# Optimization experiments

Measured on AMD Instinct MI355X. Metric: run time of the kernel, lower is better.

The kernel has to match this reference:

```python
import jax, jax.numpy as jnp
import numpy as np

NUM_HEADS = 16
HEAD_DIM = 64
D_MODEL = 1024
OUTPUT_DIM = 1024


def setup_inputs() -> dict:
    key = jax.random.key(0)
    ks = jax.random.split(key, 11)
    B, S, H = 2, 2048, D_MODEL
    inner = NUM_HEADS * HEAD_DIM
    s = 0.02
    return {
        "query": jax.random.normal(ks[0], (B, S, H), jnp.float32),
        "key": jax.random.normal(ks[1], (B, S, H), jnp.float32),
        "value": jax.random.normal(ks[2], (B, S, H), jnp.float32),
        "Wq": jax.random.normal(ks[3], (H, inner), jnp.float32) * s,
        "bq": jnp.zeros((inner,), jnp.float32),
        "Wk": jax.random.normal(ks[4], (H, inner), jnp.float32) * s,
        "bk": jnp.zeros((inner,), jnp.float32),
        "Wv": jax.random.normal(ks[5], (H, inner), jnp.float32) * s,
        "bv": jnp.zeros((inner,), jnp.float32),
        "Wo": jax.random.normal(ks[6], (inner, OUTPUT_DIM), jnp.float32) * s,
        "bo": jnp.zeros((OUTPUT_DIM,), jnp.float32),
    }


def reference(query, key, value, Wq, bq, Wk, bk, Wv, bv, Wo, bo):
    B, Sq, _ = query.shape
    Sk = key.shape[1]
    nh, dh = NUM_HEADS, HEAD_DIM
    # projections -> [B, S, nh, dh]
    Q = (query @ Wq + bq).reshape(B, Sq, nh, dh)
    K = (key @ Wk + bk).reshape(B, Sk, nh, dh)
    V = (value @ Wv + bv).reshape(B, Sk, nh, dh)
    # scores [B, nh, Sq, Sk]
    scores = jnp.einsum("bqhd,bkhd->bhqk", Q, K) / jnp.sqrt(jnp.float32(dh))
    attn = jax.nn.softmax(scores, axis=-1)
    out = jnp.einsum("bhqk,bkhd->bqhd", attn, V).reshape(B, Sq, nh * dh)
    return out @ Wo + bo
```

## Files before the change

kernel.cpp:

```cpp
#include <hip/hip_runtime.h>
#include <math.h>

typedef __attribute__((ext_vector_type(8))) short short8;
typedef __attribute__((ext_vector_type(4))) short short4v;
typedef __attribute__((ext_vector_type(4))) float f32x4;
typedef __attribute__((ext_vector_type(2))) float f32x2;

#if __has_builtin(__builtin_amdgcn_mfma_f32_16x16x16bf16_1k)
#define HAVE_MFMA16 1
#else
#define HAVE_MFMA16 0
#endif

__device__ __forceinline__ short f2bf(float f) {
  union { float f; unsigned u; } x; x.f = f;
  unsigned r = x.u + 0x7fffu + ((x.u >> 16) & 1u);
  return (short)(r >> 16);
}
#if __has_builtin(__builtin_amdgcn_cvt_pk_bf16_f32)
typedef __attribute__((ext_vector_type(2))) __bf16 bf16x2;
__device__ __forceinline__ unsigned pack_bf(float a, float b) {
  union { bf16x2 v; unsigned u; } t;
  t.v = __builtin_amdgcn_cvt_pk_bf16_f32(a, b);
  return t.u;
}
#else
__device__ __forceinline__ unsigned pack_bf(float a, float b) {
  union { float f; unsigned u; } x, y; x.f = a; y.f = b;
  unsigned ra = x.u + 0x7fffu + ((x.u >> 16) & 1u);
  unsigned rb = y.u + 0x7fffu + ((y.u >> 16) & 1u);
  return (ra >> 16) | (rb & 0xffff0000u);
}
#endif
__device__ __forceinline__ float fast_exp2(float x) {
#if __has_builtin(__builtin_amdgcn_exp2f)
  return __builtin_amdgcn_exp2f(x);
#else
  return exp2f(x);
#endif
}
union U4S8 { unsigned u[4]; short8 s; };
union U2S4 { unsigned u[2]; short4v s; };

__device__ __forceinline__ void async16(const short* g, short* lds_uniform) {
  __builtin_amdgcn_global_load_lds(
      (const __attribute__((address_space(1))) void*)g,
      (__attribute__((address_space(3))) void*)lds_uniform, 16, 0, 0);
}

__global__ __launch_bounds__(256) void wconv(
    const float* __restrict__ W0, const float* __restrict__ W1,
    const float* __restrict__ W2, const float* __restrict__ W3,
    short* __restrict__ T0, short* __restrict__ T1,
    short* __restrict__ T2, short* __restrict__ T3) {
  const float* W; short* T;
  switch (blockIdx.z) {
    case 0: W = W0; T = T0; break;
    case 1: W = W1; T = T1; break;
    case 2: W = W2; T = T2; break;
    default: W = W3; T = T3; break;
  }
  __shared__ __align__(16) short t[64][72];
  const int tid = threadIdx.x;
  const int x0 = blockIdx.x * 64, y0 = blockIdx.y * 64;
  {
    int rr = tid >> 2, cc = (tid & 3) * 16;
    const float* p = W + (size_t)(x0 + rr) * 1024 + y0 + cc;
    f32x4 v[4];
    v[0] = *(const f32x4*)(p + 0);  v[1] = *(const f32x4*)(p + 4);
    v[2] = *(const f32x4*)(p + 8);  v[3] = *(const f32x4*)(p + 12);
#pragma unroll
    for (int i = 0; i < 4; ++i)
#pragma unroll
      for (int j = 0; j < 4; ++j)
        t[cc + 4 * i + j][rr] = f2bf(v[i][j]);
  }
  __syncthreads();
  {
    int nr = tid >> 2, kc = (tid & 3) * 16;
    short* q = T + (size_t)(y0 + nr) * 1024 + x0 + kc;
    *(short8*)q       = *(const short8*)&t[nr][kc];
    *(short8*)(q + 8) = *(const short8*)&t[nr][kc + 8];
  }
}

__global__ __launch_bounds__(256) void aconv(
    const float* __restrict__ X0, const float* __restrict__ X1, const float* __restrict__ X2,
    short* __restrict__ Y0, short* __restrict__ Y1, short* __restrict__ Y2) {
  const float* X; short* Y;
  switch (blockIdx.z) {
    case 0: X = X0; Y = Y0; break;
    case 1: X = X1; Y = Y1; break;
    default: X = X2; Y = Y2; break;
  }
  size_t idx = ((size_t)blockIdx.x * 256 + threadIdx.x) * 16;
  f32x4 v0 = *(const f32x4*)(X + idx + 0);
  f32x4 v1 = *(const f32x4*)(X + idx + 4);
  f32x4 v2 = *(const f32x4*)(X + idx + 8);
  f32x4 v3 = *(const f32x4*)(X + idx + 12);
  U4S8 a, b;
  a.u[0] = pack_bf(v0[0], v0[1]); a.u[1] = pack_bf(v0[2], v0[3]);
  a.u[2] = pack_bf(v1[0], v1[1]); a.u[3] = pack_bf(v1[2], v1[3]);
  b.u[0] = pack_bf(v2[0], v2[1]); b.u[1] = pack_bf(v2[2], v2[3]);
  b.u[2] = pack_bf(v3[0], v3[1]); b.u[3] = pack_bf(v3[2], v3[3]);
  *(short8*)(Y + idx) = a.s;
  *(short8*)(Y + idx + 8) = b.s;
}

template <bool OUT_F32, int BM>
__global__ __launch_bounds__(256) void gemm_async(
    const short* __restrict__ A0, const short* __restrict__ A1, const short* __restrict__ A2,
    const short* __restrict__ B0, const short* __restrict__ B1, const short* __restrict__ B2,
    const float* __restrict__ b0, const float* __restrict__ b1, const float* __restrict__ b2,
    void* __restrict__ C0, void* __restrict__ C1, void* __restrict__ C2,
    float s0, float s1, float s2, int M, int N, int K) {
  const int z = blockIdx.z;
  const short* A    = z == 0 ? A0 : (z == 1 ? A1 : A2);
  const short* B    = z == 0 ? B0 : (z == 1 ? B1 : B2);
  const float* bias = z == 0 ? b0 : (z == 1 ? b1 : b2);
  void*        Cv   = z == 0 ? C0 : (z == 1 ? C1 : C2);
  const float  cs   = z == 0 ? s0 : (z == 1 ? s1 : s2);

  constexpr int MF = BM / 32;
  constexpr int AJ = BM / 64;
  __shared__ __align__(16) short As[BM * 32];
  __shared__ __align__(16) short Bs[128 * 32];
  const int tid = threadIdx.x;
  const int l = tid & 63, w = tid >> 6;
  const int lr = l & 15, lq = l >> 4;
  const int lin = blockIdx.x + (int)gridDim.x * blockIdx.y;
  const int ny = (int)gridDim.y;
  const int yb = lin % ny, xb = lin / ny;
  const int m0 = yb * BM, n0 = xb * 128;
  const int wm = (w >> 1) * (BM / 2), wn = (w & 1) * 64;
  f32x4 acc[MF][4] = {};

  const int lrow = l >> 2, lcol = (l & 3) * 8;
  const short* aptr[AJ];
  short* alds[AJ];
#pragma unroll
  for (int j = 0; j < AJ; ++j) {
    int chunk = w * AJ + j;
    aptr[j] = A + (size_t)(m0 + chunk * 16 + lrow) * K + lcol;
    alds[j] = &As[chunk * 512];
  }
  const short* bptr[2];
  short* blds[2];
#pragma unroll
  for (int j = 0; j < 2; ++j) {
    int chunk = w * 2 + j;
    bptr[j] = B + (size_t)(n0 + chunk * 16 + lrow) * K + lcol;
    blds[j] = &Bs[chunk * 512];
  }

  const int KT = K >> 5;
  for (int kt = 0; kt < KT; ++kt) {
    const int k0 = kt * 32;
    __syncthreads();
#pragma unroll
    for (int j = 0; j < AJ; ++j) async16(aptr[j] + k0, alds[j]);
#pragma unroll
    for (int j = 0; j < 2; ++j) async16(bptr[j] + k0, blds[j]);
    __syncthreads();

    short8 af[MF], bfr[4];
#pragma unroll
    for (int i = 0; i < MF; ++i)
      af[i] = *(const short8*)&As[(wm + i * 16 + lr) * 32 + lq * 8];
#pragma unroll
    for (int i = 0; i < 4; ++i)
      bfr[i] = *(const short8*)&Bs[(wn + i * 16 + lr) * 32 + lq * 8];
#pragma unroll
    for (int mi = 0; mi < MF; ++mi)
#pragma unroll
      for (int ni = 0; ni < 4; ++ni)
        acc[mi][ni] = __builtin_amdgcn_mfma_f32_16x16x32_bf16(af[mi], bfr[ni], acc[mi][ni], 0, 0, 0);
  }

#pragma unroll
  for (int ni = 0; ni < 4; ++ni) {
    int gn = n0 + wn + ni * 16 + lr;
    float bv = bias[gn];
#pragma unroll
    for (int mi = 0; mi < MF; ++mi) {
      int gm = m0 + wm + mi * 16 + lq * 4;
#pragma unroll
      for (int r = 0; r < 4; ++r) {
        float val = (acc[mi][ni][r] + bv) * cs;
        if constexpr (OUT_F32)
          ((float*)Cv)[(size_t)(gm + r) * N + gn] = val;
        else
          ((short*)Cv)[(size_t)(gm + r) * N + gn] = f2bf(val);
      }
    }
  }
}

template <bool A_IS_F32, bool B_IS_BF16, bool OUT_F32, int BM>
__global__ __launch_bounds__(256) void gemm_bias(
    const void* __restrict__ A0, const void* __restrict__ A1, const void* __restrict__ A2,
    const void* __restrict__ B0, const void* __restrict__ B1, const void* __restrict__ B2,
    const float* __restrict__ b0, const float* __restrict__ b1, const float* __restrict__ b2,
    void* __restrict__ C0, void* __restrict__ C1, void* __restrict__ C2,
    float s0, float s1, float s2, int M, int N, int K) {
  const int z = blockIdx.z;
  const void*  Av   = z == 0 ? A0 : (z == 1 ? A1 : A2);
  const void*  Bv   = z == 0 ? B0 : (z == 1 ? B1 : B2);
  const float* bias = z == 0 ? b0 : (z == 1 ? b1 : b2);
  void*        Cv   = z == 0 ? C0 : (z == 1 ? C1 : C2);
  const float  cs   = z == 0 ? s0 : (z == 1 ? s1 : s2);

  constexpr int MF = BM / 32;
  __shared__ __align__(16) short As[BM * 40];
  __shared__ __align__(16) short Bs[128 * 40];
  const int tid = threadIdx.x;
  const int l = tid & 63, w = tid >> 6;
  const int lr = l & 15, lq = l >> 4;
  const int lin = blockIdx.x + (int)gridDim.x * blockIdx.y;
  const int ny = (int)gridDim.y;
  const int yb = lin % ny, xb = lin / ny;
  const int m0 = yb * BM, n0 = xb * 128;
  const int wm = (w >> 1) * (BM / 2), wn = (w & 1) * 64;
  f32x4 acc[MF][4] = {};

  constexpr int TPR = 256 / BM;
  const int ar = tid / TPR, ac = (tid % TPR) * (32 / TPR);
  const int br = tid >> 1, bcc = (tid & 1) * 16;
  const int dp = tid & 63, kb = tid >> 6;

  f32x4 avf[MF];
  short8 avb[BM / 64 > 0 ? BM / 64 : 1];
  short8 bvb[2];
  f32x2 bvf[8];

  auto load_regs = [&](int k0) {
    if constexpr (A_IS_F32) {
      const float* Ap = (const float*)Av + (size_t)(m0 + ar) * K + k0 + ac;
#pragma unroll
      for (int i = 0; i < MF; ++i) avf[i] = *(const f32x4*)(Ap + 4 * i);
    } else {
      const short* Ap = (const short*)Av + (size_t)(m0 + ar) * K + k0 + ac;
#pragma unroll
      for (int i = 0; i < BM / 64; ++i) avb[i] = *(const short8*)(Ap + 8 * i);
    }
    if constexpr (B_IS_BF16) {
      const short* Bp = (const short*)Bv + (size_t)(n0 + br) * K + k0 + bcc;
      bvb[0] = *(const short8*)(Bp + 0);
      bvb[1] = *(const short8*)(Bp + 8);
    } else {
      const float* Bp = (const float*)Bv + (size_t)(k0 + kb * 8) * N + n0 + 2 * dp;
#pragma unroll
      for (int i = 0; i < 4; ++i) {
        bvf[2 * i]     = *(const f32x2*)(Bp + (size_t)(2 * i) * N);
        bvf[2 * i + 1] = *(const f32x2*)(Bp + (size_t)(2 * i + 1) * N);
      }
    }
  };
  auto write_lds = [&]() {
    if constexpr (A_IS_F32) {
#pragma unroll
      for (int j = 0; j < MF / 2; ++j) {
        U4S8 p;
        p.u[0] = pack_bf(avf[2 * j][0], avf[2 * j][1]);
        p.u[1] = pack_bf(avf[2 * j][2], avf[2 * j][3]);
        p.u[2] = pack_bf(avf[2 * j + 1][0], avf[2 * j + 1][1]);
        p.u[3] = pack_bf(avf[2 * j + 1][2], avf[2 * j + 1][3]);
        *(short8*)&As[ar * 40 + ac + 8 * j] = p.s;
      }
    } else {
#pragma unroll
      for (int j = 0; j < BM / 64; ++j)
        *(short8*)&As[ar * 40 + ac + 8 * j] = avb[j];
    }
    if constexpr (B_IS_BF16) {
      *(short8*)&Bs[br * 40 + bcc] = bvb[0];
      *(short8*)&Bs[br * 40 + bcc + 8] = bvb[1];
    } else {
      U4S8 lo, hi;
#pragma unroll
      for (int i = 0; i < 4; ++i) {
        lo.u[i] = pack_bf(bvf[2 * i][0], bvf[2 * i + 1][0]);
        hi.u[i] = pack_bf(bvf[2 * i][1], bvf[2 * i + 1][1]);
      }
      *(short8*)&Bs[(2 * dp) * 40 + kb * 8] = lo.s;
      *(short8*)&Bs[(2 * dp + 1) * 40 + kb * 8] = hi.s;
    }
  };

  load_regs(0);
  const int KT = K >> 5;
  for (int kt = 0; kt < KT; ++kt) {
    write_lds();
    __syncthreads();
    if (kt + 1 < KT) load_regs((kt + 1) * 32);

    short8 af[MF], bfr[4];
#pragma unroll
    for (int i = 0; i < MF; ++i)
      af[i] = *(const short8*)&As[(wm + i * 16 + lr) * 40 + lq * 8];
#pragma unroll
    for (int i = 0; i < 4; ++i)
      bfr[i] = *(const short8*)&Bs[(wn + i * 16 + lr) * 40 + lq * 8];
#pragma unroll
    for (int mi = 0; mi < MF; ++mi)
#pragma unroll
      for (int ni = 0; ni < 4; ++ni)
        acc[mi][ni] = __builtin_amdgcn_mfma_f32_16x16x32_bf16(af[mi], bfr[ni], acc[mi][ni], 0, 0, 0);
    __syncthreads();
  }

#pragma unroll
  for (int ni = 0; ni < 4; ++ni) {
    int gn = n0 + wn + ni * 16 + lr;
    float bv = bias[gn];
#pragma unroll
    for (int mi = 0; mi < MF; ++mi) {
      int gm = m0 + wm + mi * 16 + lq * 4;
#pragma unroll
      for (int r = 0; r < 4; ++r) {
        float val = (acc[mi][ni][r] + bv) * cs;
        if constexpr (OUT_F32)
          ((float*)Cv)[(size_t)(gm + r) * N + gn] = val;
        else
          ((short*)Cv)[(size_t)(gm + r) * N + gn] = f2bf(val);
      }
    }
  }
}

__global__ __launch_bounds__(256) void attn128(
    const short* __restrict__ Q, const short* __restrict__ K,
    const short* __restrict__ V, short* __restrict__ ctx) {
  __shared__ __align__(16) short Ks[64][72];
  __shared__ __align__(16) short Vt[64][72];
#if !HAVE_MFMA16
  __shared__ __align__(16) short Ps2[4][32][68];
#endif
  const int tid = threadIdx.x, l = tid & 63, w = tid >> 6;
  const int lr = l & 15, lq = l >> 4;
  const int lin = blockIdx.x + 16 * blockIdx.y;
  const int h = lin & 15, qblk = lin >> 4;
  const int b = blockIdx.z, q0 = qblk * 128;
  const size_t bh = (size_t)b * 2048 * 1024 + (size_t)h * 64;
  const short* Kg = K + bh;
  const short* Vg = V + bh;

  short8 qb[2][2];
#pragma unroll
  for (int qf = 0; qf < 2; ++qf)
#pragma unroll
    for (int ks = 0; ks < 2; ++ks)
      qb[qf][ks] = *(const short8*)&Q[bh + (size_t)(q0 + w * 32 + qf * 16 + lr) * 1024 + ks * 32 + lq * 8];

  f32x4 accO[4][2] = {};
  float lpart[2] = {0.f, 0.f};

  const int kr = tid >> 2, kc = (tid & 3) * 16;
  const int vdp = tid & 31, vkb = tid >> 5;

  short8 kv0, kv1;
  unsigned vu[8];
  auto load_kv = [&](int kt) {
    const short* Kp = &Kg[(size_t)(kt * 64 + kr) * 1024 + kc];
    kv0 = *(const short8*)(Kp + 0);
    kv1 = *(const short8*)(Kp + 8);
#pragma unroll
    for (int i = 0; i < 8; ++i)
      vu[i] = *(const unsigned*)&Vg[(size_t)(kt * 64 + vkb * 8 + i) * 1024 + vdp * 2];
  };
  auto write_kv = [&]() {
    *(short8*)&Ks[kr][kc] = kv0;
    *(short8*)&Ks[kr][kc + 8] = kv1;
    U4S8 lo, hi;
#pragma unroll
    for (int j = 0; j < 4; ++j) {
      lo.u[j] = (vu[2 * j] & 0xffffu) | (vu[2 * j + 1] << 16);
      hi.u[j] = (vu[2 * j] >> 16) | (vu[2 * j + 1] & 0xffff0000u);
    }
    *(short8*)&Vt[2 * vdp][vkb * 8] = lo.s;
    *(short8*)&Vt[2 * vdp + 1][vkb * 8] = hi.s;
  };

  load_kv(0);
  for (int kt = 0; kt < 32; ++kt) {
    write_kv();
    __syncthreads();
    if (kt + 1 < 32) load_kv(kt + 1);

    short8 ka[4][2];
#pragma unroll
    for (int ni = 0; ni < 4; ++ni)
#pragma unroll
      for (int ks = 0; ks < 2; ++ks)
        ka[ni][ks] = *(const short8*)&Ks[ni * 16 + lr][ks * 32 + lq * 8];
    f32x4 s[4][2] = {};
#pragma unroll
    for (int ni = 0; ni < 4; ++ni)
#pragma unroll
      for (int qf = 0; qf < 2; ++qf) {
        s[ni][qf] = __builtin_amdgcn_mfma_f32_16x16x32_bf16(ka[ni][0], qb[qf][0], s[ni][qf], 0, 0, 0);
        s[ni][qf] = __builtin_amdgcn_mfma_f32_16x16x32_bf16(ka[ni][1], qb[qf][1], s[ni][qf], 0, 0, 0);
      }

    unsigned pk[4][2][2];
#pragma unroll
    for (int ni = 0; ni < 4; ++ni)
#pragma unroll
      for (int qf = 0; qf < 2; ++qf) {
        float p0 = fast_exp2(s[ni][qf][0]);
        float p1 = fast_exp2(s[ni][qf][1]);
        float p2 = fast_exp2(s[ni][qf][2]);
        float p3 = fast_exp2(s[ni][qf][3]);
        lpart[qf] += (p0 + p1) + (p2 + p3);
        pk[ni][qf][0] = pack_bf(p0, p1);
        pk[ni][qf][1] = pack_bf(p2, p3);
      }

#if HAVE_MFMA16
#pragma unroll
    for (int di = 0; di < 4; ++di)
#pragma unroll
      for (int ni = 0; ni < 4; ++ni) {
        short4v vb = *(const short4v*)&Vt[di * 16 + lr][ni * 16 + lq * 4];
#pragma unroll
        for (int qf = 0; qf < 2; ++qf) {
          U2S4 a; a.u[0] = pk[ni][qf][0]; a.u[1] = pk[ni][qf][1];
          accO[di][qf] = __builtin_amdgcn_mfma_f32_16x16x16bf16_1k(a.s, vb, accO[di][qf], 0, 0, 0);
        }
      }
#else
#pragma unroll
    for (int ni = 0; ni < 4; ++ni)
#pragma unroll
      for (int qf = 0; qf < 2; ++qf) {
        unsigned* dst = (unsigned*)&Ps2[w][qf * 16 + lr][16 * ni + 4 * lq];
        dst[0] = pk[ni][qf][0];
        dst[1] = pk[ni][qf][1];
      }
#pragma unroll
    for (int ks = 0; ks < 2; ++ks)
#pragma unroll
      for (int qf = 0; qf < 2; ++qf) {
        const short* src = &Ps2[w][qf * 16 + lr][32 * ks + 8 * lq];
        U4S8 a;
        a.u[0] = ((const unsigned*)src)[0]; a.u[1] = ((const unsigned*)src)[1];
        a.u[2] = ((const unsigned*)src)[2]; a.u[3] = ((const unsigned*)src)[3];
#pragma unroll
        for (int di = 0; di < 4; ++di) {
          short8 vb = *(const short8*)&Vt[di * 16 + lr][ks * 32 + lq * 8];
          accO[di][qf] = __builtin_amdgcn_mfma_f32_16x16x32_bf16(a.s, vb, accO[di][qf], 0, 0, 0);
        }
      }
#endif
    __syncthreads();
  }

#pragma unroll
  for (int qf = 0; qf < 2; ++qf) {
    lpart[qf] += __shfl_xor(lpart[qf], 16, 64);
    lpart[qf] += __shfl_xor(lpart[qf], 32, 64);
  }
  float inv[2] = {1.0f / lpart[0], 1.0f / lpart[1]};
  float ir[2][4];
#pragma unroll
  for (int qf = 0; qf < 2; ++qf)
#pragma unroll
    for (int r = 0; r < 4; ++r)
      ir[qf][r] = __shfl(inv[qf], 4 * lq + r, 64);

#pragma unroll
  for (int qf = 0; qf < 2; ++qf)
#pragma unroll
    for (int r = 0; r < 4; ++r) {
      size_t row = bh + (size_t)(q0 + w * 32 + qf * 16 + 4 * lq + r) * 1024;
#pragma unroll
      for (int di = 0; di < 4; ++di)
        ctx[row + di * 16 + lr] = f2bf(accO[di][qf][r] * ir[qf][r]);
    }
}

extern "C" void kernel_launch(void* const* d_in, const int* in_sizes, int n_in,
                              void* d_out, int out_size, void* d_ws, size_t ws_size,
                              hipStream_t stream) {
  const void*  query = d_in[0];
  const void*  key   = d_in[1];
  const void*  value = d_in[2];
  const float* Wq = (const float*)d_in[3];
  const float* bq = (const float*)d_in[4];
  const float* Wk = (const float*)d_in[5];
  const float* bk = (const float*)d_in[6];
  const float* Wv = (const float*)d_in[7];
  const float* bv = (const float*)d_in[8];
  const float* Wo = (const float*)d_in[9];
  const float* bo = (const float*)d_in[10];

  short* ws = (short*)d_ws;
  const size_t MT = 4096ull * 1024ull;
  const size_t WSZ = 1024ull * 1024ull;
  const float qscale = 0.125f * 1.4426950408889634f;

  short* Qb = ws;
  short* Vb = ws + MT;
  short* Kb = (short*)d_out;

  const bool turbo = ws_size >= (4 * MT + 4 * WSZ) * sizeof(short);

  if (turbo) {
    short* Qcv = ws + 2 * MT;
    short* Vcv = ws + 3 * MT;
    short* Kcv = (short*)d_out + MT;
    short* WqT = ws + 4 * MT;
    short* WkT = WqT + WSZ;
    short* WvT = WqT + 2 * WSZ;
    short* WoT = WqT + 3 * WSZ;

    wconv<<<dim3(16, 16, 4), 256, 0, stream>>>(Wq, Wk, Wv, Wo, WqT, WkT, WvT, WoT);
    aconv<<<dim3(1024, 1, 3), 256, 0, stream>>>(
        (const float*)query, (const float*)key, (const float*)value, Qcv, Kcv, Vcv);
    gemm_async<false, 128><<<dim3(8, 32, 3), 256, 0, stream>>>(
        Qcv, Kcv, Vcv, WqT, WkT, WvT, bq, bk, bv, Qb, Kb, Vb,
        qscale, 1.0f, 1.0f, 4096, 1024, 1024);
    attn128<<<dim3(16, 16, 2), 256, 0, stream>>>(Qb, Kb, Vb, Qb);
    gemm_async<true, 64><<<dim3(8, 64, 1), 256, 0, stream>>>(
        Qb, Qb, Qb, WoT, WoT, WoT, bo, bo, bo, d_out, d_out, d_out,
        1.0f, 1.0f, 1.0f, 4096, 1024, 1024);
    return;
  }

  const bool roomy = ws_size >= (2 * MT + 4 * WSZ) * sizeof(short);
  short *WqT, *WkT, *WvT, *WoT;
  if (roomy) {
    short* base = ws + 2 * MT;
    WqT = base; WkT = base + WSZ; WvT = base + 2 * WSZ; WoT = base + 3 * WSZ;
  } else {
    short* tail = (short*)d_out + MT;
    WqT = tail; WkT = tail + WSZ; WvT = tail + 2 * WSZ; WoT = nullptr;
  }

  wconv<<<dim3(16, 16, roomy ? 4 : 3), 256, 0, stream>>>(
      Wq, Wk, Wv, Wo, WqT, WkT, WvT, roomy ? WoT : WvT);

  gemm_bias<true, true, false, 128><<<dim3(8, 32, 3), 256, 0, stream>>>(
      query, key, value, WqT, WkT, WvT, bq, bk, bv, Qb, Kb, Vb,
      qscale, 1.0f, 1.0f, 4096, 1024, 1024);

  attn128<<<dim3(16, 16, 2), 256, 0, stream>>>(Qb, Kb, Vb, Qb);

  if (roomy)
    gemm_bias<false, true, true, 64><<<dim3(8, 64, 1), 256, 0, stream>>>(
        Qb, Qb, Qb, WoT, WoT, WoT, bo, bo, bo, d_out, d_out, d_out,
        1.0f, 1.0f, 1.0f, 4096, 1024, 1024);
  else
    gemm_bias<false, false, true, 64><<<dim3(8, 64, 1), 256, 0, stream>>>(
        Qb, Qb, Qb, Wo, Wo, Wo, bo, bo, bo, d_out, d_out, d_out,
        1.0f, 1.0f, 1.0f, 4096, 1024, 1024);
}
```

Measured before the change: 240.3 us.

## Halve attention query tile to 64 rows and swizzle transposed V in LDS

The attention kernel now gives each block 64 query rows instead of 128, so each wave owns a single 16-row fragment, and launches twice as many blocks (1024 instead of 512). It also XOR-style rotates the column placement of the transposed V tile in shared memory to cut bank conflicts on both the writes and the MFMA operand reads. More blocks improve occupancy and load balance across CUs and lower register pressure. In exchange, K/V tiles are loaded and transposed twice as often per query row, doubling global and LDS traffic per unit of compute.

```diff
diff --git a/kernel.cpp b/kernel.cpp
--- a/kernel.cpp
+++ b/kernel.cpp
@@ -328,35 +328,34 @@
   }
 }
 
-__global__ __launch_bounds__(256) void attn128(
+__global__ __launch_bounds__(256) void attn64(
     const short* __restrict__ Q, const short* __restrict__ K,
     const short* __restrict__ V, short* __restrict__ ctx) {
   __shared__ __align__(16) short Ks[64][72];
   __shared__ __align__(16) short Vt[64][72];
 #if !HAVE_MFMA16
-  __shared__ __align__(16) short Ps2[4][32][68];
+  __shared__ __align__(16) short Ps2[4][16][68];
 #endif
   const int tid = threadIdx.x, l = tid & 63, w = tid >> 6;
   const int lr = l & 15, lq = l >> 4;
-  const int lin = blockIdx.x + 16 * blockIdx.y;
+  const int lin = blockIdx.x + 32 * blockIdx.y;
   const int h = lin & 15, qblk = lin >> 4;
-  const int b = blockIdx.z, q0 = qblk * 128;
+  const int b = blockIdx.z, q0 = qblk * 64;
   const size_t bh = (size_t)b * 2048 * 1024 + (size_t)h * 64;
   const short* Kg = K + bh;
   const short* Vg = V + bh;
 
-  short8 qb[2][2];
-#pragma unroll
-  for (int qf = 0; qf < 2; ++qf)
-#pragma unroll
-    for (int ks = 0; ks < 2; ++ks)
-      qb[qf][ks] = *(const short8*)&Q[bh + (size_t)(q0 + w * 32 + qf * 16 + lr) * 1024 + ks * 32 + lq * 8];
-
-  f32x4 accO[4][2] = {};
-  float lpart[2] = {0.f, 0.f};
+  short8 qb[2];
+#pragma unroll
+  for (int ks = 0; ks < 2; ++ks)
+    qb[ks] = *(const short8*)&Q[bh + (size_t)(q0 + w * 16 + lr) * 1024 + ks * 32 + lq * 8];
+
+  f32x4 accO[4] = {};
+  float lpart = 0.f;
 
   const int kr = tid >> 2, kc = (tid & 3) * 16;
   const int vdp = tid & 31, vkb = tid >> 5;
+  const int vswz = ((vkb + (vdp >> 2)) & 7) * 8;
 
   short8 kv0, kv1;
   unsigned vu[8];
@@ -377,8 +376,8 @@
       lo.u[j] = (vu[2 * j] & 0xffffu) | (vu[2 * j + 1] << 16);
       hi.u[j] = (vu[2 * j] >> 16) | (vu[2 * j + 1] & 0xffff0000u);
     }
-    *(short8*)&Vt[2 * vdp][vkb * 8] = lo.s;
-    *(short8*)&Vt[2 * vdp + 1][vkb * 8] = hi.s;
+    *(short8*)&Vt[2 * vdp][vswz] = lo.s;
+    *(short8*)&Vt[2 * vdp + 1][vswz] = hi.s;
   };
 
   load_kv(0);
@@ -393,90 +392,79 @@
 #pragma unroll
       for (int ks = 0; ks < 2; ++ks)
         ka[ni][ks] = *(const short8*)&Ks[ni * 16 + lr][ks * 32 + lq * 8];
-    f32x4 s[4][2] = {};
-#pragma unroll
-    for (int ni = 0; ni < 4; ++ni)
-#pragma unroll
-      for (int qf = 0; qf < 2; ++qf) {
-        s[ni][qf] = __builtin_amdgcn_mfma_f32_16x16x32_bf16(ka[ni][0], qb[qf][0], s[ni][qf], 0, 0, 0);
-        s[ni][qf] = __builtin_amdgcn_mfma_f32_16x16x32_bf16(ka[ni][1], qb[qf][1], s[ni][qf], 0, 0, 0);
-      }
-
-    unsigned pk[4][2][2];
-#pragma unroll
-    for (int ni = 0; ni < 4; ++ni)
-#pragma unroll
-      for (int qf = 0; qf < 2; ++qf) {
-        float p0 = fast_exp2(s[ni][qf][0]);
-        float p1 = fast_exp2(s[ni][qf][1]);
-        float p2 = fast_exp2(s[ni][qf][2]);
-        float p3 = fast_exp2(s[ni][qf][3]);
-        lpart[qf] += (p0 + p1) + (p2 + p3);
-        pk[ni][qf][0] = pack_bf(p0, p1);
-        pk[ni][qf][1] = pack_bf(p2, p3);
-      }
+    f32x4 s[4] = {};
+#pragma unroll
+    for (int ni = 0; ni < 4; ++ni) {
+      s[ni] = __builtin_amdgcn_mfma_f32_16x16x32_bf16(ka[ni][0], qb[0], s[ni], 0, 0, 0);
+      s[ni] = __builtin_amdgcn_mfma_f32_16x16x32_bf16(ka[ni][1], qb[1], s[ni], 0, 0, 0);
+    }
+
+    unsigned pk[4][2];
+#pragma unroll
+    for (int ni = 0; ni < 4; ++ni) {
+      float p0 = fast_exp2(s[ni][0]);
+      float p1 = fast_exp2(s[ni][1]);
+      float p2 = fast_exp2(s[ni][2]);
+      float p3 = fast_exp2(s[ni][3]);
+      lpart += (p0 + p1) + (p2 + p3);
+      pk[ni][0] = pack_bf(p0, p1);
+      pk[ni][1] = pack_bf(p2, p3);
+    }
 
 #if HAVE_MFMA16
 #pragma unroll
-    for (int di = 0; di < 4; ++di)
+    for (int di = 0; di < 4; ++di) {
+      const int dR = di * 16 + lr;
+      const int ud = 2 * di + (lr >> 3);
 #pragma unroll
       for (int ni = 0; ni < 4; ++ni) {
-        short4v vb = *(const short4v*)&Vt[di * 16 + lr][ni * 16 + lq * 4];
-#pragma unroll
-        for (int qf = 0; qf < 2; ++qf) {
-          U2S4 a; a.u[0] = pk[ni][qf][0]; a.u[1] = pk[ni][qf][1];
-          accO[di][qf] = __builtin_amdgcn_mfma_f32_16x16x16bf16_1k(a.s, vb, accO[di][qf], 0, 0, 0);
-        }
-      }
+        const int pb = ((2 * ni + (lq >> 1) + ud) & 7) * 8 + (lq & 1) * 4;
+        short4v vb = *(const short4v*)&Vt[dR][pb];
+        U2S4 a; a.u[0] = pk[ni][0]; a.u[1] = pk[ni][1];
+        accO[di] = __builtin_amdgcn_mfma_f32_16x16x16bf16_1k(a.s, vb, accO[di], 0, 0, 0);
+      }
+    }
 #else
 #pragma unroll
-    for (int ni = 0; ni < 4; ++ni)
-#pragma unroll
-      for (int qf = 0; qf < 2; ++qf) {
-        unsigned* dst = (unsigned*)&Ps2[w][qf * 16 + lr][16 * ni + 4 * lq];
-        dst[0] = pk[ni][qf][0];
-        dst[1] = pk[ni][qf][1];
-      }
-#pragma unroll
-    for (int ks = 0; ks < 2; ++ks)
-#pragma unroll
-      for (int qf = 0; qf < 2; ++qf) {
-        const short* src = &Ps2[w][qf * 16 + lr][32 * ks + 8 * lq];
-        U4S8 a;
-        a.u[0] = ((const unsigned*)src)[0]; a.u[1] = ((const unsigned*)src)[1];
-        a.u[2] = ((const unsigned*)src)[2]; a.u[3] = ((const unsigned*)src)[3];
-#pragma unroll
-        for (int di = 0; di < 4; ++di) {
-          short8 vb = *(const short8*)&Vt[di * 16 + lr][ks * 32 + lq * 8];
-          accO[di][qf] = __builtin_amdgcn_mfma_f32_16x16x32_bf16(a.s, vb, accO[di][qf], 0, 0, 0);
-        }
-      }
+    for (int ni = 0; ni < 4; ++ni) {
+      unsigned* dst = (unsigned*)&Ps2[w][lr][16 * ni + 4 * lq];
+      dst[0] = pk[ni][0];
+      dst[1] = pk[ni][1];
+    }
+#pragma unroll
+    for (int ks = 0; ks < 2; ++ks) {
+      const short* src = &Ps2[w][lr][32 * ks + 8 * lq];
+      U4S8 a;
+      a.u[0] = ((const unsigned*)src)[0]; a.u[1] = ((const unsigned*)src)[1];
+      a.u[2] = ((const unsigned*)src)[2]; a.u[3] = ((const unsigned*)src)[3];
+#pragma unroll
+      for (int di = 0; di < 4; ++di) {
+        const int dR = di * 16 + lr;
+        const int ud = 2 * di + (lr >> 3);
+        const int pb = ((4 * ks + lq + ud) & 7) * 8;
+        short8 vb = *(const short8*)&Vt[dR][pb];
+        accO[di] = __builtin_amdgcn_mfma_f32_16x16x32_bf16(a.s, vb, accO[di], 0, 0, 0);
+      }
+    }
 #endif
     __syncthreads();
   }
 
-#pragma unroll
-  for (int qf = 0; qf < 2; ++qf) {
-    lpart[qf] += __shfl_xor(lpart[qf], 16, 64);
-    lpart[qf] += __shfl_xor(lpart[qf], 32, 64);
-  }
-  float inv[2] = {1.0f / lpart[0], 1.0f / lpart[1]};
-  float ir[2][4];
-#pragma unroll
-  for (int qf = 0; qf < 2; ++qf)
-#pragma unroll
-    for (int r = 0; r < 4; ++r)
-      ir[qf][r] = __shfl(inv[qf], 4 * lq + r, 64);
-
-#pragma unroll
-  for (int qf = 0; qf < 2; ++qf)
-#pragma unroll
-    for (int r = 0; r < 4; ++r) {
-      size_t row = bh + (size_t)(q0 + w * 32 + qf * 16 + 4 * lq + r) * 1024;
-#pragma unroll
-      for (int di = 0; di < 4; ++di)
-        ctx[row + di * 16 + lr] = f2bf(accO[di][qf][r] * ir[qf][r]);
-    }
+  lpart += __shfl_xor(lpart, 16, 64);
+  lpart += __shfl_xor(lpart, 32, 64);
+  float inv = 1.0f / lpart;
+  float ir[4];
+#pragma unroll
+  for (int r = 0; r < 4; ++r)
+    ir[r] = __shfl(inv, 4 * lq + r, 64);
+
+#pragma unroll
+  for (int r = 0; r < 4; ++r) {
+    size_t row = bh + (size_t)(q0 + w * 16 + 4 * lq + r) * 1024;
+#pragma unroll
+    for (int di = 0; di < 4; ++di)
+      ctx[row + di * 16 + lr] = f2bf(accO[di][r] * ir[r]);
+  }
 }
 
 extern "C" void kernel_launch(void* const* d_in, const int* in_sizes, int n_in,
@@ -520,7 +508,7 @@
     gemm_async<false, 128><<<dim3(8, 32, 3), 256, 0, stream>>>(
         Qcv, Kcv, Vcv, WqT, WkT, WvT, bq, bk, bv, Qb, Kb, Vb,
         qscale, 1.0f, 1.0f, 4096, 1024, 1024);
-    attn128<<<dim3(16, 16, 2), 256, 0, stream>>>(Qb, Kb, Vb, Qb);
+    attn64<<<dim3(32, 16, 2), 256, 0, stream>>>(Qb, Kb, Vb, Qb);
     gemm_async<true, 64><<<dim3(8, 64, 1), 256, 0, stream>>>(
         Qb, Qb, Qb, WoT, WoT, WoT, bo, bo, bo, d_out, d_out, d_out,
         1.0f, 1.0f, 1.0f, 4096, 1024, 1024);
@@ -544,7 +532,7 @@
       query, key, value, WqT, WkT, WvT, bq, bk, bv, Qb, Kb, Vb,
       qscale, 1.0f, 1.0f, 4096, 1024, 1024);
 
-  attn128<<<dim3(16, 16, 2), 256, 0, stream>>>(Qb, Kb, Vb, Qb);
+  attn64<<<dim3(32, 16, 2), 256, 0, stream>>>(Qb, Kb, Vb, Qb);
 
   if (roomy)
     gemm_bias<false, true, true, 64><<<dim3(8, 64, 1), 256, 0, stream>>>(
```

After: 248.9 us. +3.6%, slower.

## Double-buffer K/V shared tiles in attention and swizzle transposed V layout

Applied to the files above, without the earlier changes.

The attention kernel now keeps two shared-memory buffers for the K and transposed V tiles and alternates between them each iteration. This removes the trailing barrier per key tile. The transposed V writes and reads also use an XOR-like rotation of 8-element column groups to reduce LDS bank conflicts on the V-fragment loads. The cost is double the shared memory for K/V (about 36KB), which may lower occupancy.

```diff
diff --git a/kernel.cpp b/kernel.cpp
--- a/kernel.cpp
+++ b/kernel.cpp
@@ -328,11 +328,11 @@
   }
 }
 
-__global__ __launch_bounds__(256) void attn128(
+__global__ __launch_bounds__(256) void attn128db(
     const short* __restrict__ Q, const short* __restrict__ K,
     const short* __restrict__ V, short* __restrict__ ctx) {
-  __shared__ __align__(16) short Ks[64][72];
-  __shared__ __align__(16) short Vt[64][72];
+  __shared__ __align__(16) short Ks[2][64][72];
+  __shared__ __align__(16) short Vt[2][64][72];
 #if !HAVE_MFMA16
   __shared__ __align__(16) short Ps2[4][32][68];
 #endif
@@ -357,6 +357,7 @@
 
   const int kr = tid >> 2, kc = (tid & 3) * 16;
   const int vdp = tid & 31, vkb = tid >> 5;
+  const int vswz = ((vkb + (vdp >> 2)) & 7) * 8;
 
   short8 kv0, kv1;
   unsigned vu[8];
@@ -368,22 +369,23 @@
     for (int i = 0; i < 8; ++i)
       vu[i] = *(const unsigned*)&Vg[(size_t)(kt * 64 + vkb * 8 + i) * 1024 + vdp * 2];
   };
-  auto write_kv = [&]() {
-    *(short8*)&Ks[kr][kc] = kv0;
-    *(short8*)&Ks[kr][kc + 8] = kv1;
+  auto write_kv = [&](int buf) {
+    *(short8*)&Ks[buf][kr][kc] = kv0;
+    *(short8*)&Ks[buf][kr][kc + 8] = kv1;
     U4S8 lo, hi;
 #pragma unroll
     for (int j = 0; j < 4; ++j) {
       lo.u[j] = (vu[2 * j] & 0xffffu) | (vu[2 * j + 1] << 16);
       hi.u[j] = (vu[2 * j] >> 16) | (vu[2 * j + 1] & 0xffff0000u);
     }
-    *(short8*)&Vt[2 * vdp][vkb * 8] = lo.s;
-    *(short8*)&Vt[2 * vdp + 1][vkb * 8] = hi.s;
+    *(short8*)&Vt[buf][2 * vdp][vswz] = lo.s;
+    *(short8*)&Vt[buf][2 * vdp + 1][vswz] = hi.s;
   };
 
   load_kv(0);
   for (int kt = 0; kt < 32; ++kt) {
-    write_kv();
+    const int buf = kt & 1;
+    write_kv(buf);
     __syncthreads();
     if (kt + 1 < 32) load_kv(kt + 1);
 
@@ -392,7 +394,7 @@
     for (int ni = 0; ni < 4; ++ni)
 #pragma unroll
       for (int ks = 0; ks < 2; ++ks)
-        ka[ni][ks] = *(const short8*)&Ks[ni * 16 + lr][ks * 32 + lq * 8];
+        ka[ni][ks] = *(const short8*)&Ks[buf][ni * 16 + lr][ks * 32 + lq * 8];
     f32x4 s[4][2] = {};
 #pragma unroll
     for (int ni = 0; ni < 4; ++ni)
@@ -418,16 +420,20 @@
 
 #if HAVE_MFMA16
 #pragma unroll
-    for (int di = 0; di < 4; ++di)
+    for (int di = 0; di < 4; ++di) {
+      const int dR = di * 16 + lr;
+      const int ud = 2 * di + (lr >> 3);
 #pragma unroll
       for (int ni = 0; ni < 4; ++ni) {
-        short4v vb = *(const short4v*)&Vt[di * 16 + lr][ni * 16 + lq * 4];
+        const int pb = ((2 * ni + (lq >> 1) + ud) & 7) * 8 + (lq & 1) * 4;
+        short4v vb = *(const short4v*)&Vt[buf][dR][pb];
 #pragma unroll
         for (int qf = 0; qf < 2; ++qf) {
           U2S4 a; a.u[0] = pk[ni][qf][0]; a.u[1] = pk[ni][qf][1];
           accO[di][qf] = __builtin_amdgcn_mfma_f32_16x16x16bf16_1k(a.s, vb, accO[di][qf], 0, 0, 0);
         }
       }
+    }
 #else
 #pragma unroll
     for (int ni = 0; ni < 4; ++ni)
@@ -447,12 +453,14 @@
         a.u[2] = ((const unsigned*)src)[2]; a.u[3] = ((const unsigned*)src)[3];
 #pragma unroll
         for (int di = 0; di < 4; ++di) {
-          short8 vb = *(const short8*)&Vt[di * 16 + lr][ks * 32 + lq * 8];
+          const int dR = di * 16 + lr;
+          const int ud = 2 * di + (lr >> 3);
+          const int pb = ((4 * ks + lq + ud) & 7) * 8;
+          short8 vb = *(const short8*)&Vt[buf][dR][pb];
           accO[di][qf] = __builtin_amdgcn_mfma_f32_16x16x32_bf16(a.s, vb, accO[di][qf], 0, 0, 0);
         }
       }
 #endif
-    __syncthreads();
   }
 
 #pragma unroll
@@ -520,7 +528,7 @@
     gemm_async<false, 128><<<dim3(8, 32, 3), 256, 0, stream>>>(
         Qcv, Kcv, Vcv, WqT, WkT, WvT, bq, bk, bv, Qb, Kb, Vb,
         qscale, 1.0f, 1.0f, 4096, 1024, 1024);
-    attn128<<<dim3(16, 16, 2), 256, 0, stream>>>(Qb, Kb, Vb, Qb);
+    attn128db<<<dim3(16, 16, 2), 256, 0, stream>>>(Qb, Kb, Vb, Qb);
     gemm_async<true, 64><<<dim3(8, 64, 1), 256, 0, stream>>>(
         Qb, Qb, Qb, WoT, WoT, WoT, bo, bo, bo, d_out, d_out, d_out,
         1.0f, 1.0f, 1.0f, 4096, 1024, 1024);
@@ -544,7 +552,7 @@
       query, key, value, WqT, WkT, WvT, bq, bk, bv, Qb, Kb, Vb,
       qscale, 1.0f, 1.0f, 4096, 1024, 1024);
 
-  attn128<<<dim3(16, 16, 2), 256, 0, stream>>>(Qb, Kb, Vb, Qb);
+  attn128db<<<dim3(16, 16, 2), 256, 0, stream>>>(Qb, Kb, Vb, Qb);
 
   if (roomy)
     gemm_bias<false, true, true, 64><<<dim3(8, 64, 1), 256, 0, stream>>>(
```

New measurement: 238.9 us. Within noise of the previous version (-0.6%).
